# Performance work log

Measured on AMD Instinct MI355X. Metric: run time of the kernel, lower is better.

Reference implementation:

```python
import jax, jax.numpy as jnp
import numpy as np

H = 16      # num_heads
DH = 64     # dim_heads


def rotate_half(x):
    # '... (j d) -> ... j d', j=2; unbind -> (x1, x2); cat(-x2, x1)
    x1, x2 = jnp.split(x, 2, axis=-1)
    return jnp.concatenate([-x2, x1], axis=-1)


def apply_rope(t, freqs):
    # t: [b, h, s, d], freqs: [s, d] (rot_dim == d, so no unrotated tail)
    return t * jnp.cos(freqs) + rotate_half(t) * jnp.sin(freqs)


def setup_inputs() -> dict:
    key = jax.random.key(0)
    k1, k2, k3, k4 = jax.random.split(key, 4)
    B, S, D = 2, 2048, 1024
    x = jax.random.normal(k1, (B, S, D), dtype=jnp.float32)
    w_qkv = jax.random.normal(k2, (D, 3 * D), dtype=jnp.float32) * (D ** -0.5)
    w_out = jax.random.normal(k3, (D, D), dtype=jnp.float32) * (D ** -0.5)
    freqs = jax.random.normal(k4, (S, DH), dtype=jnp.float32)
    return {"x": x, "w_qkv": w_qkv, "w_out": w_out, "freqs": freqs}


def reference(x, w_qkv, w_out, freqs):
    B, S, D = x.shape
    qkv = x @ w_qkv                                   # [B, S, 3D]
    q, k, v = jnp.split(qkv, 3, axis=-1)
    def to_heads(t):
        return t.reshape(B, S, H, DH).transpose(0, 2, 1, 3)  # [B, H, S, DH]
    q, k, v = map(to_heads, (q, k, v))
    # rotary (computed in float32, which is already the working dtype)
    q = apply_rope(q, freqs)
    k = apply_rope(k, freqs)
    # causal SDPA, scale = 1/sqrt(dh)
    scale = DH ** -0.5
    scores = jnp.einsum('bhqd,bhkd->bhqk', q, k) * scale
    causal_mask = jnp.tril(jnp.ones((S, S), dtype=bool))
    scores = jnp.where(causal_mask, scores, jnp.finfo(scores.dtype).min)
    attn = jax.nn.softmax(scores, axis=-1)
    out = jnp.einsum('bhqk,bhkd->bhqd', attn, v)      # [B, H, S, DH]
    out = out.transpose(0, 2, 1, 3).reshape(B, S, D)  # 'b h n d -> b n (h d)'
    return out @ w_out
```

## Files before the change

### kernel.cpp

```cpp
#include <hip/hip_runtime.h>


typedef __bf16 bf16x8 __attribute__((ext_vector_type(8)));
typedef float f32x4 __attribute__((ext_vector_type(4)));

__device__ __forceinline__ unsigned short f2b(float f) {
  unsigned int u = __builtin_bit_cast(unsigned int, f);
  unsigned int lsb = (u >> 16) & 1u;
  u += 0x7fffu + lsb;
  return (unsigned short)(u >> 16);
}
__device__ __forceinline__ float b2f(unsigned short h) {
  unsigned int u = ((unsigned int)h) << 16;
  return __builtin_bit_cast(float, u);
}
__device__ __forceinline__ unsigned int pk2(float a, float b) {
  return (unsigned int)f2b(a) | ((unsigned int)f2b(b) << 16);
}
__device__ __forceinline__ unsigned int cvtpk(float lo, float hi) {
  unsigned int r;
  asm("v_cvt_pk_bf16_f32 %0, %1, %2" : "=v"(r) : "v"(lo), "v"(hi));
  return r;
}
__device__ __forceinline__ void unp8(uint4 v, float* f) {
  unsigned int u[4] = {v.x, v.y, v.z, v.w};
#pragma unroll
  for (int i = 0; i < 4; ++i) {
    f[2 * i] = b2f((unsigned short)(u[i] & 0xffff));
    f[2 * i + 1] = b2f((unsigned short)(u[i] >> 16));
  }
}
__device__ __forceinline__ void gload16(const void* g, void* l) {
  __builtin_amdgcn_global_load_lds(
      (const __attribute__((address_space(1))) unsigned int*)g,
      (__attribute__((address_space(3))) unsigned int*)l, 16, 0, 0);
}

__global__ __launch_bounds__(256) void prologue_kernel(
    const float* __restrict__ x, unsigned short* __restrict__ xb,
    const float* __restrict__ freqs, float* __restrict__ cosT,
    float* __restrict__ sinT, const float* __restrict__ w_qkv,
    unsigned short* __restrict__ wqT, const float* __restrict__ w_out,
    unsigned short* __restrict__ woT) {
  __shared__ float tile[32][33];
  const int blk = blockIdx.x, tid = threadIdx.x;

  if (blk < 4096) {
    int i = (blk * 256 + tid) * 4;
    float4 v = *(const float4*)&x[i];
    ushort4 o;
    o.x = f2b(v.x); o.y = f2b(v.y); o.z = f2b(v.z); o.w = f2b(v.w);
    *(ushort4*)&xb[i] = o;
    return;
  }
  if (blk < 4608) {
    int i = (blk - 4096) * 256 + tid;
    float f = freqs[i];
    cosT[i] = cosf(f);
    sinT[i] = sinf(f);
    return;
  }
  const float* src;
  unsigned short* dst;
  int K, N, bx, by;
  if (blk < 7680) {
    src = w_qkv; dst = wqT; K = 1024; N = 3072;
    const int t = blk - 4608;
    bx = t % 96; by = t / 96;
  } else {
    src = w_out; dst = woT; K = 1024; N = 1024;
    const int t = blk - 7680;
    bx = t % 32; by = t / 32;
  }
  const int n0 = bx * 32, k0 = by * 32;
  const int c = tid & 31, r4 = tid >> 5;
#pragma unroll
  for (int p = 0; p < 4; ++p) {
    int r = r4 + p * 8;
    tile[r][c] = src[(size_t)(k0 + r) * N + n0 + c];
  }
  __syncthreads();
#pragma unroll
  for (int p = 0; p < 4; ++p) {
    int r = r4 + p * 8;
    dst[(size_t)(n0 + r) * K + k0 + c] = f2b(tile[c][r]);
  }
}

__global__ __launch_bounds__(256, 2) void gemm_wide(const unsigned short* __restrict__ A,
                                                    const unsigned short* __restrict__ BT,
                                                    unsigned short* __restrict__ C,
                                                    int M, int N, int K) {
  extern __shared__ unsigned short L[];
  const int tid = threadIdx.x, lane = tid & 63, w = tid >> 6;
  const int wr = w >> 1, wc = w & 1;
  const int fr = lane & 15, oct = lane >> 4;

  const int m0 = blockIdx.y * 128, n0 = blockIdx.x * 192;

  const int sr = tid >> 2;
  const int scol = ((tid & 3) ^ ((tid >> 3) & 3)) * 8;
  const size_t aR0 = (size_t)(m0 + sr) * K + scol;
  const size_t aR1 = (size_t)(m0 + 64 + sr) * K + scol;
  const size_t bR0 = (size_t)(n0 + sr) * K + scol;
  const size_t bR1 = (size_t)(n0 + 64 + sr) * K + scol;
  const size_t bR2 = (size_t)(n0 + 128 + sr) * K + scol;

  f32x4 acc[4][6] = {};
  const int T = K >> 5;

  for (int pt = 0; pt < 3; ++pt) {
    unsigned short* Ln = &L[pt * 10240];
    const size_t gk = (size_t)pt * 32;
    gload16(&A[aR0 + gk], &Ln[tid * 8]);
    gload16(&A[aR1 + gk], &Ln[2048 + tid * 8]);
    gload16(&BT[bR0 + gk], &Ln[4096 + tid * 8]);
    gload16(&BT[bR1 + gk], &Ln[6144 + tid * 8]);
    gload16(&BT[bR2 + gk], &Ln[8192 + tid * 8]);
  }

  for (int t = 0; t < T; ++t) {
    if (t + 3 <= T) {
      asm volatile("s_waitcnt vmcnt(10)" ::: "memory");
    } else if (t + 2 == T) {
      asm volatile("s_waitcnt vmcnt(5)" ::: "memory");
    } else {
      asm volatile("s_waitcnt vmcnt(0)" ::: "memory");
    }
    __builtin_amdgcn_sched_barrier(0);
    __builtin_amdgcn_s_barrier();
    __builtin_amdgcn_sched_barrier(0);

    const unsigned short* Lb = &L[(t & 3) * 10240];
    unsigned short* Ln = &L[((t + 3) & 3) * 10240];
    const size_t gk = (size_t)(t + 3) * 32;
    const bool doStage = (t + 3 < T);

    bf16x8 af[4], bf[6];
#pragma unroll
    for (int i = 0; i < 4; ++i) {
      const int ra = wr * 64 + i * 16 + fr;
      af[i] = __builtin_bit_cast(
          bf16x8, *(const uint4*)&Lb[ra * 32 + ((oct ^ ((ra >> 1) & 3)) * 8)]);
    }
#pragma unroll
    for (int j = 0; j < 3; ++j) {
      const int rb = wc * 96 + j * 16 + fr;
      bf[j] = __builtin_bit_cast(
          bf16x8,
          *(const uint4*)&Lb[4096 + rb * 32 + ((oct ^ ((rb >> 1) & 3)) * 8)]);
    }
    if (doStage) {
      gload16(&A[aR0 + gk], &Ln[tid * 8]);
      gload16(&A[aR1 + gk], &Ln[2048 + tid * 8]);
      gload16(&BT[bR0 + gk], &Ln[4096 + tid * 8]);
    }
    __builtin_amdgcn_s_setprio(1);
#pragma unroll
    for (int i = 0; i < 4; ++i)
#pragma unroll
      for (int j = 0; j < 3; ++j)
        acc[i][j] = __builtin_amdgcn_mfma_f32_16x16x32_bf16(af[i], bf[j], acc[i][j], 0, 0, 0);
    __builtin_amdgcn_s_setprio(0);

#pragma unroll
    for (int j = 3; j < 6; ++j) {
      const int rb = wc * 96 + j * 16 + fr;
      bf[j] = __builtin_bit_cast(
          bf16x8,
          *(const uint4*)&Lb[4096 + rb * 32 + ((oct ^ ((rb >> 1) & 3)) * 8)]);
    }
    if (doStage) {
      gload16(&BT[bR1 + gk], &Ln[6144 + tid * 8]);
      gload16(&BT[bR2 + gk], &Ln[8192 + tid * 8]);
    }
    __builtin_amdgcn_s_setprio(1);
#pragma unroll
    for (int i = 0; i < 4; ++i)
#pragma unroll
      for (int j = 3; j < 6; ++j)
        acc[i][j] = __builtin_amdgcn_mfma_f32_16x16x32_bf16(af[i], bf[j], acc[i][j], 0, 0, 0);
    __builtin_amdgcn_s_setprio(0);
  }

#pragma unroll
  for (int i = 0; i < 4; ++i)
#pragma unroll
    for (int j = 0; j < 6; ++j)
#pragma unroll
      for (int r = 0; r < 4; ++r)
        C[(size_t)(m0 + wr * 64 + i * 16 + oct * 4 + r) * N + n0 + wc * 96 +
          j * 16 + fr] = f2b(acc[i][j][r]);
}

__global__ __launch_bounds__(256, 2) void gemm2_ring(const unsigned short* __restrict__ A,
                                                     const unsigned short* __restrict__ BT,
                                                     float* __restrict__ C,
                                                     int M, int N, int K) {
  extern __shared__ unsigned short L[];
  const int tid = threadIdx.x, lane = tid & 63, w = tid >> 6;
  const int wr = w >> 1, wc = w & 1;
  const int fr = lane & 15, oct = lane >> 4;
  const int m0 = blockIdx.y * 128, n0 = blockIdx.x * 64;

  const int sr = tid >> 2;
  const int scol = ((tid & 3) ^ ((tid >> 3) & 3)) * 8;
  const size_t aR0 = (size_t)(m0 + sr) * K + scol;
  const size_t aR1 = (size_t)(m0 + 64 + sr) * K + scol;
  const size_t bR0 = (size_t)(n0 + sr) * K + scol;

  f32x4 acc[4][2] = {};
  const int T = K >> 5;

  for (int pt = 0; pt < 3; ++pt) {
    unsigned short* Ln = &L[pt * 6144];
    const size_t gk = (size_t)pt * 32;
    gload16(&A[aR0 + gk], &Ln[tid * 8]);
    gload16(&A[aR1 + gk], &Ln[2048 + tid * 8]);
    gload16(&BT[bR0 + gk], &Ln[4096 + tid * 8]);
  }

  for (int t = 0; t < T; ++t) {
    if (t + 3 <= T) {
      asm volatile("s_waitcnt vmcnt(6)" ::: "memory");
    } else if (t + 2 == T) {
      asm volatile("s_waitcnt vmcnt(3)" ::: "memory");
    } else {
      asm volatile("s_waitcnt vmcnt(0)" ::: "memory");
    }
    __builtin_amdgcn_sched_barrier(0);
    __builtin_amdgcn_s_barrier();
    __builtin_amdgcn_sched_barrier(0);

    const unsigned short* Lb = &L[(t & 3) * 6144];
    unsigned short* Ln = &L[((t + 3) & 3) * 6144];
    const size_t gk = (size_t)(t + 3) * 32;
    const bool doStage = (t + 3 < T);

    bf16x8 af[4], bq[2];
#pragma unroll
    for (int i = 0; i < 4; ++i) {
      const int ra = wr * 64 + i * 16 + fr;
      af[i] = __builtin_bit_cast(
          bf16x8, *(const uint4*)&Lb[ra * 32 + ((oct ^ ((ra >> 1) & 3)) * 8)]);
    }
#pragma unroll
    for (int j = 0; j < 2; ++j) {
      const int rb = wc * 32 + j * 16 + fr;
      bq[j] = __builtin_bit_cast(
          bf16x8,
          *(const uint4*)&Lb[4096 + rb * 32 + ((oct ^ ((rb >> 1) & 3)) * 8)]);
    }
    if (doStage) {
      gload16(&A[aR0 + gk], &Ln[tid * 8]);
      gload16(&A[aR1 + gk], &Ln[2048 + tid * 8]);
      gload16(&BT[bR0 + gk], &Ln[4096 + tid * 8]);
    }
    __builtin_amdgcn_s_setprio(1);
#pragma unroll
    for (int i = 0; i < 4; ++i)
#pragma unroll
      for (int j = 0; j < 2; ++j)
        acc[i][j] = __builtin_amdgcn_mfma_f32_16x16x32_bf16(af[i], bq[j], acc[i][j], 0, 0, 0);
    __builtin_amdgcn_s_setprio(0);
  }

#pragma unroll
  for (int i = 0; i < 4; ++i)
#pragma unroll
    for (int j = 0; j < 2; ++j)
#pragma unroll
      for (int r = 0; r < 4; ++r)
        C[(size_t)(m0 + wr * 64 + i * 16 + oct * 4 + r) * N + n0 + wc * 32 +
          j * 16 + fr] = acc[i][j][r];
}

__global__ __launch_bounds__(256) void prep_kernel(const unsigned short* __restrict__ qkvb,
                                                   const float* __restrict__ cosT,
                                                   const float* __restrict__ sinT,
                                                   unsigned short* __restrict__ Qb,
                                                   unsigned short* __restrict__ Kb,
                                                   unsigned short* __restrict__ Vtg) {
  const int sb = blockIdx.x, h = blockIdx.y, b = blockIdx.z;
  const int tid = threadIdx.x;
  __shared__ float Vs[64][65];
  const int sl = tid >> 2, c8 = (tid & 3) * 8;
  const int s = sb * 64 + sl;
  const size_t tok = (size_t)(b * 2048 + s);
  const unsigned short* row = qkvb + tok * 3072 + h * 64;
  const float QSCALE = 0.125f * 1.44269504f;

  float cl[8], snl[8], ch[8], snh[8];
  {
    const float* cb = cosT + s * 64;
    const float* sbp = sinT + s * 64;
    *(float4*)&cl[0] = *(const float4*)&cb[c8];
    *(float4*)&cl[4] = *(const float4*)&cb[c8 + 4];
    *(float4*)&ch[0] = *(const float4*)&cb[32 + c8];
    *(float4*)&ch[4] = *(const float4*)&cb[32 + c8 + 4];
    *(float4*)&snl[0] = *(const float4*)&sbp[c8];
    *(float4*)&snl[4] = *(const float4*)&sbp[c8 + 4];
    *(float4*)&snh[0] = *(const float4*)&sbp[32 + c8];
    *(float4*)&snh[4] = *(const float4*)&sbp[32 + c8 + 4];
  }
  const size_t obase = ((size_t)(b * 16 + h) * 2048 + s) * 64;

  {
    float lo[8], hi[8];
    unp8(*(const uint4*)(row + c8), lo);
    unp8(*(const uint4*)(row + 32 + c8), hi);
    float olo[8], ohi[8];
#pragma unroll
    for (int e = 0; e < 8; ++e) {
      olo[e] = (lo[e] * cl[e] - hi[e] * snl[e]) * QSCALE;
      ohi[e] = (hi[e] * ch[e] + lo[e] * snh[e]) * QSCALE;
    }
    uint4 w0, w1;
    w0.x = pk2(olo[0], olo[1]); w0.y = pk2(olo[2], olo[3]);
    w0.z = pk2(olo[4], olo[5]); w0.w = pk2(olo[6], olo[7]);
    w1.x = pk2(ohi[0], ohi[1]); w1.y = pk2(ohi[2], ohi[3]);
    w1.z = pk2(ohi[4], ohi[5]); w1.w = pk2(ohi[6], ohi[7]);
    *(uint4*)(Qb + obase + c8) = w0;
    *(uint4*)(Qb + obase + 32 + c8) = w1;
  }
  {
    float lo[8], hi[8];
    unp8(*(const uint4*)(row + 1024 + c8), lo);
    unp8(*(const uint4*)(row + 1024 + 32 + c8), hi);
    float olo[8], ohi[8];
#pragma unroll
    for (int e = 0; e < 8; ++e) {
      olo[e] = lo[e] * cl[e] - hi[e] * snl[e];
      ohi[e] = hi[e] * ch[e] + lo[e] * snh[e];
    }
    uint4 w0, w1;
    w0.x = pk2(olo[0], olo[1]); w0.y = pk2(olo[2], olo[3]);
    w0.z = pk2(olo[4], olo[5]); w0.w = pk2(olo[6], olo[7]);
    w1.x = pk2(ohi[0], ohi[1]); w1.y = pk2(ohi[2], ohi[3]);
    w1.z = pk2(ohi[4], ohi[5]); w1.w = pk2(ohi[6], ohi[7]);
    *(uint4*)(Kb + obase + c8) = w0;
    *(uint4*)(Kb + obase + 32 + c8) = w1;
  }
  {
    float lo[8], hi[8];
    unp8(*(const uint4*)(row + 2048 + c8), lo);
    unp8(*(const uint4*)(row + 2048 + 32 + c8), hi);
#pragma unroll
    for (int e = 0; e < 8; ++e) {
      Vs[sl][c8 + e] = lo[e];
      Vs[sl][32 + c8 + e] = hi[e];
    }
  }
  __syncthreads();
  {
    const int d = tid >> 2, q2 = tid & 3;
    const int m = q2 >> 1, tp = q2 & 1;
    const int sc0 = q2 * 16;
    const size_t vbase = (((size_t)(b * 16 + h) * 32 + sb) * 64 + d) * 64;
#pragma unroll
    for (int g = 0; g < 4; ++g) {
      ushort4 u;
      u.x = f2b(Vs[sc0 + g * 4 + 0][d]);
      u.y = f2b(Vs[sc0 + g * 4 + 1][d]);
      u.z = f2b(Vs[sc0 + g * 4 + 2][d]);
      u.w = f2b(Vs[sc0 + g * 4 + 3][d]);
      *(ushort4*)(Vtg + vbase + m * 32 + g * 8 + tp * 4) = u;
    }
  }
}

__global__ __launch_bounds__(512, 4) void attn_mfma(const unsigned short* __restrict__ Qb,
                                                    const unsigned short* __restrict__ Kb,
                                                    const unsigned short* __restrict__ Vtg,
                                                    unsigned short* __restrict__ attnb) {
  extern __shared__ unsigned short KV[];
  const int h = blockIdx.y, b = blockIdx.z;
  const int qt0 = blockIdx.x;
  const int qt1 = 31 - qt0;
  const int tid = threadIdx.x, lane = tid & 63, w = tid >> 6;
  const int fr = lane & 15, oct = lane >> 4;
  const int grp = w >> 2, wq = w & 3;
  const int nhA = 16 - qt0, nhB = 15 - qt0;

  const size_t bh = (size_t)(b * 16 + h);
  const unsigned short* Kbase = Kb + bh * 131072;
  const unsigned short* Vbase = Vtg + bh * 131072;

  const int qtP1 = grp ? qt1 : qt0;
  const unsigned short* Qp1 = Qb + (bh * 2048 + qtP1 * 64 + wq * 16 + fr) * 64;
  const bf16x8 qa0 = __builtin_bit_cast(bf16x8, *(const uint4*)(Qp1 + oct * 8));
  const bf16x8 qa1 = __builtin_bit_cast(bf16x8, *(const uint4*)(Qp1 + 32 + oct * 8));
  const unsigned short* Qp2 = Qb + (bh * 2048 + qt1 * 64 + wq * 16 + fr) * 64;
  const bf16x8 qb0 = __builtin_bit_cast(bf16x8, *(const uint4*)(Qp2 + oct * 8));
  const bf16x8 qb1 = __builtin_bit_cast(bf16x8, *(const uint4*)(Qp2 + 32 + oct * 8));

  float m_prev = -1e30f;
  f32x4 acc[4] = {};
  f32x4 accl = {};

  uint4 onesu;
  onesu.x = 0x3F803F80u; onesu.y = 0x3F803F80u;
  onesu.z = 0x3F803F80u; onesu.w = 0x3F803F80u;
  const bf16x8 onesf = __builtin_bit_cast(bf16x8, onesu);

  auto tile_step = [&](int buf, bf16x8 q0, bf16x8 q1, bool domask) {
    const unsigned short* Kbuf = &KV[buf * 4608];
    const unsigned short* Vbuf = &KV[(4 + buf) * 4608];
    f32x4 s4[4];
    __builtin_amdgcn_s_setprio(1);
#pragma unroll
    for (int t = 0; t < 4; ++t) {
      bf16x8 kf0 = __builtin_bit_cast(bf16x8, *(const uint4*)&Kbuf[(t * 16 + fr) * 72 + oct * 8]);
      bf16x8 kf1 = __builtin_bit_cast(bf16x8, *(const uint4*)&Kbuf[(t * 16 + fr) * 72 + 32 + oct * 8]);
      f32x4 s = {};
      s = __builtin_amdgcn_mfma_f32_16x16x32_bf16(kf0, q0, s, 0, 0, 0);
      s = __builtin_amdgcn_mfma_f32_16x16x32_bf16(kf1, q1, s, 0, 0, 0);
      s4[t] = s;
    }
    __builtin_amdgcn_s_setprio(0);
    if (domask) {
#pragma unroll
      for (int t = 0; t < 4; ++t)
#pragma unroll
        for (int r = 0; r < 4; ++r)
          if (t * 16 + oct * 4 + r > wq * 16 + fr) s4[t][r] = -1e30f;
    }

    float pm = -1e30f;
#pragma unroll
    for (int t = 0; t < 4; ++t)
#pragma unroll
      for (int r = 0; r < 4; ++r) pm = fmaxf(pm, s4[t][r]);
    const bool need = __any(pm - m_prev > 11.0f);
    if (need) {
      float pmf = fmaxf(pm, __shfl_xor(pm, 16));
      pmf = fmaxf(pmf, __shfl_xor(pmf, 32));
      float mnew = fmaxf(m_prev, pmf);
      float cf = __builtin_amdgcn_exp2f(m_prev - mnew);
      m_prev = mnew;
      float cfr[4];
#pragma unroll
      for (int r = 0; r < 4; ++r) cfr[r] = __shfl(cf, oct * 4 + r);
#pragma unroll
      for (int t2 = 0; t2 < 4; ++t2)
#pragma unroll
        for (int r = 0; r < 4; ++r) acc[t2][r] *= cfr[r];
#pragma unroll
      for (int r = 0; r < 4; ++r) accl[r] *= cfr[r];
    }
    const float mc = m_prev;
#pragma unroll
    for (int t = 0; t < 4; ++t)
#pragma unroll
      for (int r = 0; r < 4; ++r)
        s4[t][r] = __builtin_amdgcn_exp2f(s4[t][r] - mc);

    uint4 pw0, pw1;
    pw0.x = cvtpk(s4[0][0], s4[0][1]); pw0.y = cvtpk(s4[0][2], s4[0][3]);
    pw0.z = cvtpk(s4[1][0], s4[1][1]); pw0.w = cvtpk(s4[1][2], s4[1][3]);
    pw1.x = cvtpk(s4[2][0], s4[2][1]); pw1.y = cvtpk(s4[2][2], s4[2][3]);
    pw1.z = cvtpk(s4[3][0], s4[3][1]); pw1.w = cvtpk(s4[3][2], s4[3][3]);
    const bf16x8 pa0 = __builtin_bit_cast(bf16x8, pw0);
    const bf16x8 pa1 = __builtin_bit_cast(bf16x8, pw1);

    __builtin_amdgcn_s_setprio(1);
#pragma unroll
    for (int t2 = 0; t2 < 4; ++t2) {
      bf16x8 vf0 = __builtin_bit_cast(bf16x8, *(const uint4*)&Vbuf[(t2 * 16 + fr) * 72 + oct * 8]);
      bf16x8 vf1 = __builtin_bit_cast(bf16x8, *(const uint4*)&Vbuf[(t2 * 16 + fr) * 72 + 32 + oct * 8]);
      f32x4 a = acc[t2];
      a = __builtin_amdgcn_mfma_f32_16x16x32_bf16(pa0, vf0, a, 0, 0, 0);
      a = __builtin_amdgcn_mfma_f32_16x16x32_bf16(pa1, vf1, a, 0, 0, 0);
      acc[t2] = a;
    }
    {
      f32x4 a = accl;
      a = __builtin_amdgcn_mfma_f32_16x16x32_bf16(pa0, onesf, a, 0, 0, 0);
      a = __builtin_amdgcn_mfma_f32_16x16x32_bf16(pa1, onesf, a, 0, 0, 0);
      accl = a;
    }
    __builtin_amdgcn_s_setprio(0);
  };

  auto write_out = [&](int qtile) {
#pragma unroll
    for (int r = 0; r < 4; ++r) {
      float linv = 1.f / accl[r];
      size_t orow = (size_t)(b * 2048 + qtile * 64 + wq * 16 + oct * 4 + r);
#pragma unroll
      for (int t2 = 0; t2 < 4; ++t2)
        attnb[orow * 1024 + h * 64 + t2 * 16 + fr] = f2b(acc[t2][r] * linv);
    }
  };

  const int srow = tid >> 3, sc8 = (tid & 7) * 8;
  const unsigned short* kp1 = Kbase + srow * 64 + sc8;
  const unsigned short* vp1 = Vbase + srow * 64 + sc8;
  {
    uint4 kr = *(const uint4*)kp1;
    uint4 vr = *(const uint4*)vp1;
    *(uint4*)&KV[0 * 4608 + srow * 72 + sc8] = kr;
    *(uint4*)&KV[4 * 4608 + srow * 72 + sc8] = vr;
  }
  __syncthreads();

  for (int kb = 0; kb <= qt0; ++kb) {
    uint4 kr = *(const uint4*)(kp1 + (size_t)(kb + 1) * 4096);
    uint4 vr = *(const uint4*)(vp1 + (size_t)(kb + 1) * 4096);
    uint4 kr2, vr2;
    const bool extra = (kb == qt0) && (nhB > 0);
    if (extra) {
      kr2 = *(const uint4*)(kp1 + (size_t)17 * 4096);
      vr2 = *(const uint4*)(vp1 + (size_t)17 * 4096);
    }
    tile_step(kb & 1, qa0, qa1, kb == qtP1);
    const int nb = (kb + 1) & 1;
    *(uint4*)&KV[nb * 4608 + srow * 72 + sc8] = kr;
    *(uint4*)&KV[(4 + nb) * 4608 + srow * 72 + sc8] = vr;
    if (extra) {
      *(uint4*)&KV[2 * 4608 + srow * 72 + sc8] = kr2;
      *(uint4*)&KV[6 * 4608 + srow * 72 + sc8] = vr2;
    }
    __syncthreads();
  }

  if (grp == 0) {
    write_out(qt0);
    m_prev = -1e30f;
    f32x4 zz = {};
    accl = zz;
#pragma unroll
    for (int t2 = 0; t2 < 4; ++t2) acc[t2] = zz;
  }

  const int t2id = tid & 255;
  const int sk2 = t2id >> 2, sc2 = (t2id & 3) * 16;
  const int cnt = grp ? nhB : nhA;
  for (int i = 0; i < nhA; ++i) {
    const int kbm = grp ? (17 + i) : (qt0 + 1 + i);
    const int buf = grp ? (2 + (i & 1)) : (kbm & 1);
    uint4 k0, k1, v0, v1;
    const bool pf = (i + 1 < cnt);
    if (pf) {
      const unsigned short* ks = Kbase + (size_t)((kbm + 1) * 64 + sk2) * 64 + sc2;
      const unsigned short* vs = Vbase + (size_t)((kbm + 1) * 64 + sk2) * 64 + sc2;
      k0 = *(const uint4*)ks; k1 = *(const uint4*)(ks + 8);
      v0 = *(const uint4*)vs; v1 = *(const uint4*)(vs + 8);
    }
    if (i < cnt) tile_step(buf, qb0, qb1, kbm == qt1);
    if (pf) {
      const int nb = grp ? (2 + ((i + 1) & 1)) : ((kbm + 1) & 1);
      *(uint4*)&KV[nb * 4608 + sk2 * 72 + sc2] = k0;
      *(uint4*)&KV[nb * 4608 + sk2 * 72 + sc2 + 8] = k1;
      *(uint4*)&KV[(4 + nb) * 4608 + sk2 * 72 + sc2] = v0;
      *(uint4*)&KV[(4 + nb) * 4608 + sk2 * 72 + sc2 + 8] = v1;
    }
    __syncthreads();
  }

  float* MF = (float*)KV;
  if (grp == 1) {
#pragma unroll
    for (int t2 = 0; t2 < 4; ++t2)
#pragma unroll
      for (int r = 0; r < 4; ++r)
        MF[(wq * 16 + oct * 4 + r) * 68 + t2 * 16 + fr] = acc[t2][r];
    if (fr == 0) {
#pragma unroll
      for (int r = 0; r < 4; ++r) MF[4352 + wq * 16 + oct * 4 + r] = accl[r];
    }
    if (oct == 0) MF[4416 + wq * 16 + fr] = m_prev;
  }
  __syncthreads();
  if (grp == 0) {
    float mB = MF[4416 + wq * 16 + fr];
    float mS = fmaxf(m_prev, mB);
    float fA = __builtin_amdgcn_exp2f(m_prev - mS);
    float fB = __builtin_amdgcn_exp2f(mB - mS);
    float fAr[4], fBr[4];
#pragma unroll
    for (int r = 0; r < 4; ++r) {
      fAr[r] = __shfl(fA, oct * 4 + r);
      fBr[r] = __shfl(fB, oct * 4 + r);
    }
#pragma unroll
    for (int r = 0; r < 4; ++r)
      accl[r] = accl[r] * fAr[r] + MF[4352 + wq * 16 + oct * 4 + r] * fBr[r];
#pragma unroll
    for (int t2 = 0; t2 < 4; ++t2)
#pragma unroll
      for (int r = 0; r < 4; ++r)
        acc[t2][r] = acc[t2][r] * fAr[r] +
                     MF[(wq * 16 + oct * 4 + r) * 68 + t2 * 16 + fr] * fBr[r];
    write_out(qt1);
  }
}

extern "C" void kernel_launch(void* const* d_in, const int* in_sizes, int n_in,
                              void* d_out, int out_size, void* d_ws, size_t ws_size,
                              hipStream_t stream) {
  const float* x     = (const float*)d_in[0];
  const float* w_qkv = (const float*)d_in[1];
  const float* w_out = (const float*)d_in[2];
  const float* freqs = (const float*)d_in[3];
  float* out = (float*)d_out;

  char* ws = (char*)d_ws;
  unsigned short* qkvb = (unsigned short*)(ws);
  unsigned short* Qb   = (unsigned short*)(ws + 25165824);
  unsigned short* Kb   = (unsigned short*)(ws + 33554432);
  unsigned short* Vtg  = (unsigned short*)(ws + 41943040);
  unsigned short* attnb= (unsigned short*)(ws + 50331648);
  unsigned short* wqT  = (unsigned short*)(ws + 58720256);
  unsigned short* woT  = (unsigned short*)(ws + 65011712);
  unsigned short* xb   = (unsigned short*)(ws + 67108864);
  float* cosT          = (float*)(ws + 75497472);
  float* sinT          = (float*)(ws + 76021760);

  (void)hipFuncSetAttribute((const void*)gemm_wide,
                            hipFuncAttributeMaxDynamicSharedMemorySize, 81920);
  (void)hipFuncSetAttribute((const void*)gemm2_ring,
                            hipFuncAttributeMaxDynamicSharedMemorySize, 49152);
  (void)hipFuncSetAttribute((const void*)attn_mfma,
                            hipFuncAttributeMaxDynamicSharedMemorySize, 73728);

  prologue_kernel<<<8704, 256, 0, stream>>>(x, xb, freqs, cosT, sinT, w_qkv,
                                            wqT, w_out, woT);
  gemm_wide<<<dim3(16, 32), 256, 81920, stream>>>(xb, wqT, qkvb, 4096, 3072, 1024);
  prep_kernel<<<dim3(32, 16, 2), 256, 0, stream>>>(qkvb, cosT, sinT, Qb, Kb, Vtg);
  attn_mfma<<<dim3(16, 16, 2), 512, 73728, stream>>>(Qb, Kb, Vtg, attnb);
  gemm2_ring<<<dim3(16, 32), 256, 49152, stream>>>(attnb, woT, out, 4096, 1024, 1024);
}
```

Measured before the change: 103.9 us.

## Fuse RoPE, Q scaling and V transpose into the QKV GEMM epilogue

Removes the separate prep kernel and the intermediate bf16 qkv buffer. The QKV GEMM now remaps its B-fragment columns so each wave holds matching low and high halves of a head. Its epilogue applies rotary and the softmax scale to Q and K, and transposes V through LDS straight into the attention layouts. This saves a kernel launch and a full write and read of the 24MB qkv tensor. In exchange the epilogue issues scattered 2-byte stores and uncoalesced cos/sin loads, and adds block syncs for the V tiles.

Result: faster. 96.34 us (-7.3%).

```diff
diff --git a/kernel.cpp b/kernel.cpp
--- a/kernel.cpp
+++ b/kernel.cpp
@@ -21,14 +21,6 @@
   unsigned int r;
   asm("v_cvt_pk_bf16_f32 %0, %1, %2" : "=v"(r) : "v"(lo), "v"(hi));
   return r;
-}
-__device__ __forceinline__ void unp8(uint4 v, float* f) {
-  unsigned int u[4] = {v.x, v.y, v.z, v.w};
-#pragma unroll
-  for (int i = 0; i < 4; ++i) {
-    f[2 * i] = b2f((unsigned short)(u[i] & 0xffff));
-    f[2 * i + 1] = b2f((unsigned short)(u[i] >> 16));
-  }
 }
 __device__ __forceinline__ void gload16(const void* g, void* l) {
   __builtin_amdgcn_global_load_lds(
@@ -87,11 +79,13 @@
   }
 }
 
-__global__ __launch_bounds__(256, 2) void gemm_wide(const unsigned short* __restrict__ A,
-                                                    const unsigned short* __restrict__ BT,
-                                                    unsigned short* __restrict__ C,
-                                                    int M, int N, int K) {
+__global__ __launch_bounds__(256, 2) void gemm_fused(
+    const unsigned short* __restrict__ A, const unsigned short* __restrict__ BT,
+    unsigned short* __restrict__ Qb, unsigned short* __restrict__ Kbp,
+    unsigned short* __restrict__ Vtg, const float* __restrict__ cosT,
+    const float* __restrict__ sinT) {
   extern __shared__ unsigned short L[];
+  const int K = 1024;
   const int tid = threadIdx.x, lane = tid & 63, w = tid >> 6;
   const int wr = w >> 1, wc = w & 1;
   const int fr = lane & 15, oct = lane >> 4;
@@ -145,7 +139,7 @@
     }
 #pragma unroll
     for (int j = 0; j < 3; ++j) {
-      const int rb = wc * 96 + j * 16 + fr;
+      const int rb = j * 32 + wc * 16 + fr;
       bf[j] = __builtin_bit_cast(
           bf16x8,
           *(const uint4*)&Lb[4096 + rb * 32 + ((oct ^ ((rb >> 1) & 3)) * 8)]);
@@ -165,7 +159,7 @@
 
 #pragma unroll
     for (int j = 3; j < 6; ++j) {
-      const int rb = wc * 96 + j * 16 + fr;
+      const int rb = j * 32 + wc * 16 + fr;
       bf[j] = __builtin_bit_cast(
           bf16x8,
           *(const uint4*)&Lb[4096 + rb * 32 + ((oct ^ ((rb >> 1) & 3)) * 8)]);
@@ -183,14 +177,63 @@
     __builtin_amdgcn_s_setprio(0);
   }
 
-#pragma unroll
-  for (int i = 0; i < 4; ++i)
-#pragma unroll
-    for (int j = 0; j < 6; ++j)
-#pragma unroll
-      for (int r = 0; r < 4; ++r)
-        C[(size_t)(m0 + wr * 64 + i * 16 + oct * 4 + r) * N + n0 + wc * 96 +
-          j * 16 + fr] = f2b(acc[i][j][r]);
+  const float QSCALE = 0.125f * 1.44269504f;
+  unsigned short* vtile = L + wr * (64 * 66);
+#pragma unroll
+  for (int jp = 0; jp < 3; ++jp) {
+    const int gbase = n0 + jp * 64;
+    const int part = gbase >> 10;
+    const int hh = (gbase & 1023) >> 6;
+    const int dlo = wc * 16 + fr;
+    if (part < 2) {
+      unsigned short* dst = (part == 0) ? Qb : Kbp;
+      const float scale = (part == 0) ? QSCALE : 1.0f;
+#pragma unroll
+      for (int i = 0; i < 4; ++i) {
+#pragma unroll
+        for (int r = 0; r < 4; ++r) {
+          const int m = m0 + wr * 64 + i * 16 + oct * 4 + r;
+          const int bb = m >> 11, s = m & 2047;
+          const float lo = acc[i][2 * jp][r], hi = acc[i][2 * jp + 1][r];
+          const float cl = cosT[s * 64 + dlo], sl = sinT[s * 64 + dlo];
+          const float ch = cosT[s * 64 + 32 + dlo], sh = sinT[s * 64 + 32 + dlo];
+          const size_t ob = ((size_t)(bb * 16 + hh) * 2048 + s) * 64;
+          dst[ob + dlo] = f2b((lo * cl - hi * sl) * scale);
+          dst[ob + 32 + dlo] = f2b((hi * ch + lo * sh) * scale);
+        }
+      }
+    } else {
+      __syncthreads();
+#pragma unroll
+      for (int i = 0; i < 4; ++i)
+#pragma unroll
+        for (int r = 0; r < 4; ++r) {
+          const int s64 = i * 16 + oct * 4 + r;
+          vtile[s64 * 66 + dlo] = f2b(acc[i][2 * jp][r]);
+          vtile[s64 * 66 + 32 + dlo] = f2b(acc[i][2 * jp + 1][r]);
+        }
+      __syncthreads();
+      const int wrt = tid >> 7, t128 = tid & 127;
+      const int d = t128 >> 1, q2h = t128 & 1;
+      const unsigned short* tt = L + wrt * (64 * 66);
+      const int mtile = m0 + wrt * 64;
+      const int bb = mtile >> 11, sb = (mtile & 2047) >> 6;
+      const size_t vb = (((size_t)(bb * 16 + hh) * 32 + sb) * 64 + d) * 64;
+#pragma unroll
+      for (int q2 = 0; q2 < 2; ++q2) {
+        const int qq = q2h * 2 + q2;
+#pragma unroll
+        for (int g = 0; g < 4; ++g) {
+          ushort4 u;
+          u.x = tt[(qq * 16 + g * 4 + 0) * 66 + d];
+          u.y = tt[(qq * 16 + g * 4 + 1) * 66 + d];
+          u.z = tt[(qq * 16 + g * 4 + 2) * 66 + d];
+          u.w = tt[(qq * 16 + g * 4 + 3) * 66 + d];
+          *(ushort4*)&Vtg[vb + (qq >> 1) * 32 + g * 8 + (qq & 1) * 4] = u;
+        }
+      }
+    }
+  }
 }
 
 __global__ __launch_bounds__(256, 2) void gemm2_ring(const unsigned short* __restrict__ A,
@@ -273,100 +316,6 @@
       for (int r = 0; r < 4; ++r)
         C[(size_t)(m0 + wr * 64 + i * 16 + oct * 4 + r) * N + n0 + wc * 32 +
           j * 16 + fr] = acc[i][j][r];
-}
-
-__global__ __launch_bounds__(256) void prep_kernel(const unsigned short* __restrict__ qkvb,
-                                                   const float* __restrict__ cosT,
-                                                   const float* __restrict__ sinT,
-                                                   unsigned short* __restrict__ Qb,
-                                                   unsigned short* __restrict__ Kb,
-                                                   unsigned short* __restrict__ Vtg) {
-  const int sb = blockIdx.x, h = blockIdx.y, b = blockIdx.z;
-  const int tid = threadIdx.x;
-  __shared__ float Vs[64][65];
-  const int sl = tid >> 2, c8 = (tid & 3) * 8;
-  const int s = sb * 64 + sl;
-  const size_t tok = (size_t)(b * 2048 + s);
-  const unsigned short* row = qkvb + tok * 3072 + h * 64;
-  const float QSCALE = 0.125f * 1.44269504f;
-
-  float cl[8], snl[8], ch[8], snh[8];
-  {
-    const float* cb = cosT + s * 64;
-    const float* sbp = sinT + s * 64;
-    *(float4*)&cl[0] = *(const float4*)&cb[c8];
-    *(float4*)&cl[4] = *(const float4*)&cb[c8 + 4];
-    *(float4*)&ch[0] = *(const float4*)&cb[32 + c8];
-    *(float4*)&ch[4] = *(const float4*)&cb[32 + c8 + 4];
-    *(float4*)&snl[0] = *(const float4*)&sbp[c8];
-    *(float4*)&snl[4] = *(const float4*)&sbp[c8 + 4];
-    *(float4*)&snh[0] = *(const float4*)&sbp[32 + c8];
-    *(float4*)&snh[4] = *(const float4*)&sbp[32 + c8 + 4];
-  }
-  const size_t obase = ((size_t)(b * 16 + h) * 2048 + s) * 64;
-
-  {
-    float lo[8], hi[8];
-    unp8(*(const uint4*)(row + c8), lo);
-    unp8(*(const uint4*)(row + 32 + c8), hi);
-    float olo[8], ohi[8];
-#pragma unroll
-    for (int e = 0; e < 8; ++e) {
-      olo[e] = (lo[e] * cl[e] - hi[e] * snl[e]) * QSCALE;
-      ohi[e] = (hi[e] * ch[e] + lo[e] * snh[e]) * QSCALE;
-    }
-    uint4 w0, w1;
-    w0.x = pk2(olo[0], olo[1]); w0.y = pk2(olo[2], olo[3]);
-    w0.z = pk2(olo[4], olo[5]); w0.w = pk2(olo[6], olo[7]);
-    w1.x = pk2(ohi[0], ohi[1]); w1.y = pk2(ohi[2], ohi[3]);
-    w1.z = pk2(ohi[4], ohi[5]); w1.w = pk2(ohi[6], ohi[7]);
-    *(uint4*)(Qb + obase + c8) = w0;
-    *(uint4*)(Qb + obase + 32 + c8) = w1;
-  }
-  {
-    float lo[8], hi[8];
-    unp8(*(const uint4*)(row + 1024 + c8), lo);
-    unp8(*(const uint4*)(row + 1024 + 32 + c8), hi);
-    float olo[8], ohi[8];
-#pragma unroll
-    for (int e = 0; e < 8; ++e) {
-      olo[e] = lo[e] * cl[e] - hi[e] * snl[e];
-      ohi[e] = hi[e] * ch[e] + lo[e] * snh[e];
-    }
-    uint4 w0, w1;
-    w0.x = pk2(olo[0], olo[1]); w0.y = pk2(olo[2], olo[3]);
-    w0.z = pk2(olo[4], olo[5]); w0.w = pk2(olo[6], olo[7]);
-    w1.x = pk2(ohi[0], ohi[1]); w1.y = pk2(ohi[2], ohi[3]);
-    w1.z = pk2(ohi[4], ohi[5]); w1.w = pk2(ohi[6], ohi[7]);
-    *(uint4*)(Kb + obase + c8) = w0;
-    *(uint4*)(Kb + obase + 32 + c8) = w1;
-  }
-  {
-    float lo[8], hi[8];
-    unp8(*(const uint4*)(row + 2048 + c8), lo);
-    unp8(*(const uint4*)(row + 2048 + 32 + c8), hi);
-#pragma unroll
-    for (int e = 0; e < 8; ++e) {
-      Vs[sl][c8 + e] = lo[e];
-      Vs[sl][32 + c8 + e] = hi[e];
-    }
-  }
-  __syncthreads();
-  {
-    const int d = tid >> 2, q2 = tid & 3;
-    const int m = q2 >> 1, tp = q2 & 1;
-    const int sc0 = q2 * 16;
-    const size_t vbase = (((size_t)(b * 16 + h) * 32 + sb) * 64 + d) * 64;
-#pragma unroll
-    for (int g = 0; g < 4; ++g) {
-      ushort4 u;
-      u.x = f2b(Vs[sc0 + g * 4 + 0][d]);
-      u.y = f2b(Vs[sc0 + g * 4 + 1][d]);
-      u.z = f2b(Vs[sc0 + g * 4 + 2][d]);
-      u.w = f2b(Vs[sc0 + g * 4 + 3][d]);
-      *(ushort4*)(Vtg + vbase + m * 32 + g * 8 + tp * 4) = u;
-    }
-  }
 }
 
 __global__ __launch_bounds__(512, 4) void attn_mfma(const unsigned short* __restrict__ Qb,
@@ -606,7 +555,6 @@
   float* out = (float*)d_out;
 
   char* ws = (char*)d_ws;
-  unsigned short* qkvb = (unsigned short*)(ws);
   unsigned short* Qb   = (unsigned short*)(ws + 25165824);
   unsigned short* Kb   = (unsigned short*)(ws + 33554432);
   unsigned short* Vtg  = (unsigned short*)(ws + 41943040);
@@ -617,7 +565,7 @@
   float* cosT          = (float*)(ws + 75497472);
   float* sinT          = (float*)(ws + 76021760);
 
-  (void)hipFuncSetAttribute((const void*)gemm_wide,
+  (void)hipFuncSetAttribute((const void*)gemm_fused,
                             hipFuncAttributeMaxDynamicSharedMemorySize, 81920);
   (void)hipFuncSetAttribute((const void*)gemm2_ring,
                             hipFuncAttributeMaxDynamicSharedMemorySize, 49152);
@@ -626,8 +574,8 @@
 
   prologue_kernel<<<8704, 256, 0, stream>>>(x, xb, freqs, cosT, sinT, w_qkv,
                                             wqT, w_out, woT);
-  gemm_wide<<<dim3(16, 32), 256, 81920, stream>>>(xb, wqT, qkvb, 4096, 3072, 1024);
-  prep_kernel<<<dim3(32, 16, 2), 256, 0, stream>>>(qkvb, cosT, sinT, Qb, Kb, Vtg);
+  gemm_fused<<<dim3(16, 32), 256, 81920, stream>>>(xb, wqT, Qb, Kb, Vtg, cosT,
+                                                   sinT);
   attn_mfma<<<dim3(16, 16, 2), 512, 73728, stream>>>(Qb, Kb, Vtg, attnb);
   gemm2_ring<<<dim3(16, 32), 256, 49152, stream>>>(attnb, woT, out, 4096, 1024, 1024);
 }
```
